# Kernel optimization log

Hardware: AMD Instinct MI355X
Metric: run time of the kernel (lower is better)

Reference implementation:

```python
import jax, jax.numpy as jnp
import numpy as np

RATIO = 2          # Activation1d up_ratio = down_ratio = 2
FIR_K = 12         # up_kernel_size = down_kernel_size = 12
DN = ('NCH', 'OIH', 'NCH')


def kaiser_sinc_filter1d(cutoff, half_width, K):
    # Faithful port of BigVGAN's kaiser_sinc_filter1d (numpy, computed once at setup).
    even = (K % 2 == 0)
    half = K // 2
    delta_f = 4.0 * half_width
    A = 2.285 * (half - 1) * np.pi * delta_f + 7.95
    if A > 50.0:
        beta = 0.1102 * (A - 8.7)
    elif A >= 21.0:
        beta = 0.5842 * (A - 21.0) ** 0.4 + 0.07886 * (A - 21.0)
    else:
        beta = 0.0
    win = np.kaiser(K, beta)  # == torch.kaiser_window(K, beta, periodic=False)
    time = (np.arange(-half, half) + 0.5) if even else (np.arange(K) - half)
    filt = 2.0 * cutoff * win * np.sinc(2.0 * cutoff * time)
    filt = filt / filt.sum()
    return filt.astype(np.float32)


def snake_beta(x, log_alpha, log_beta):
    # SnakeBeta with alpha_logscale=True: x + 1/(beta+eps) * sin(alpha*x)^2
    alpha = jnp.exp(log_alpha)[None, :, None]
    beta = jnp.exp(log_beta)[None, :, None]
    return x + (1.0 / (beta + 1e-9)) * jnp.square(jnp.sin(x * alpha))


def upsample1d(x, filt):
    # UpSample1d: replicate pad, depthwise conv_transpose (stride=ratio), crop.
    C = x.shape[1]
    K = filt.shape[0]
    pad = K // RATIO - 1
    pad_left = pad * RATIO + (K - RATIO) // 2
    pad_right = pad * RATIO + (K - RATIO + 1) // 2
    xp = jnp.pad(x, ((0, 0), (0, 0), (pad, pad)), mode='edge')
    # conv_transpose == correlation with flipped kernel, lhs_dilation=stride, full padding
    w = jnp.broadcast_to(filt[::-1][None, None, :], (C, 1, K))
    y = RATIO * jax.lax.conv_general_dilated(
        xp, w, window_strides=(1,), padding=((K - 1, K - 1),),
        lhs_dilation=(RATIO,), feature_group_count=C, dimension_numbers=DN)
    return y[..., pad_left:-pad_right]  # length = 2*T


def downsample1d(x, filt):
    # DownSample1d / LowPassFilter1d: replicate pad, depthwise strided conv.
    C = x.shape[1]
    K = filt.shape[0]
    even = int(K % 2 == 0)
    pad_left = K // 2 - even
    pad_right = K // 2
    xp = jnp.pad(x, ((0, 0), (0, 0), (pad_left, pad_right)), mode='edge')
    w = jnp.broadcast_to(filt[None, None, :], (C, 1, K))
    return jax.lax.conv_general_dilated(
        xp, w, window_strides=(RATIO,), padding='VALID',
        feature_group_count=C, dimension_numbers=DN)  # length back to T


def activation1d(x, log_alpha, log_beta, up_filt, down_filt):
    return downsample1d(snake_beta(upsample1d(x, up_filt), log_alpha, log_beta), down_filt)


def conv1d_same(x, w, b, dilation):
    K = w.shape[-1]
    pad = (K - 1) * dilation // 2  # get_padding(kernel_size, dilation)
    y = jax.lax.conv_general_dilated(
        x, w, window_strides=(1,), padding=((pad, pad),),
        rhs_dilation=(dilation,), dimension_numbers=DN)
    return y + b[None, :, None]


def setup_inputs() -> dict:
    key = jax.random.key(0)
    ks = jax.random.split(key, 8)
    B, C, T, KSZ = 8, 512, 8192, 3
    x = jax.random.normal(ks[0], (B, C, T), dtype=jnp.float32)
    # SnakeBeta params (logscale init is zeros in torch; small randn for nontrivial grads)
    a1_alpha = 0.2 * jax.random.normal(ks[1], (C,), dtype=jnp.float32)
    a1_beta = 0.2 * jax.random.normal(ks[2], (C,), dtype=jnp.float32)
    a2_alpha = 0.2 * jax.random.normal(ks[3], (C,), dtype=jnp.float32)
    a2_beta = 0.2 * jax.random.normal(ks[4], (C,), dtype=jnp.float32)
    # Conv weights: init_weights -> normal(0, 0.01)
    c1_w = 0.01 * jax.random.normal(ks[5], (C, C, KSZ), dtype=jnp.float32)
    c2_w = 0.01 * jax.random.normal(ks[6], (C, C, KSZ), dtype=jnp.float32)
    c1_b = jnp.zeros((C,), dtype=jnp.float32)
    c2_b = jnp.zeros((C,), dtype=jnp.float32)
    # Kaiser-sinc low-pass FIR (cutoff=0.5/ratio, half_width=0.6/ratio) - fixed buffers
    filt = jnp.asarray(kaiser_sinc_filter1d(0.5 / RATIO, 0.6 / RATIO, FIR_K))
    return {'x': x, 'a1_alpha': a1_alpha, 'a1_beta': a1_beta,
            'a2_alpha': a2_alpha, 'a2_beta': a2_beta,
            'c1_w': c1_w, 'c1_b': c1_b, 'c2_w': c2_w, 'c2_b': c2_b,
            'up_filter': filt, 'down_filter': filt}


def reference(x, a1_alpha, a1_beta, a2_alpha, a2_beta,
              c1_w, c1_b, c2_w, c2_b, up_filter, down_filter):
    # AMPBlock0.forward: single (c1, c2, a1, a2) group; both convs dilation=1.
    xt = activation1d(x, a1_alpha, a1_beta, up_filter, down_filter)
    xt = conv1d_same(xt, c1_w, c1_b, dilation=1)
    xt = activation1d(xt, a2_alpha, a2_beta, up_filter, down_filter)
    xt = conv1d_same(xt, c2_w, c2_b, dilation=1)
    return xt + x  # lengths match, so x[:, :, :xt.shape[2]] == x
```

## Files before the change

kernel.cpp:

```cpp
#include <hip/hip_runtime.h>
#include <cstdint>
#include <cstddef>

#define B_ 8
#define C_ 512
#define T_ 8192

typedef unsigned short ushort_t;
typedef __attribute__((ext_vector_type(8))) short short8;
typedef __attribute__((ext_vector_type(8))) unsigned short ushort8_t;
typedef __attribute__((ext_vector_type(4))) float floatx4;
typedef __attribute__((ext_vector_type(4))) unsigned int uintx4;

__device__ __forceinline__ ushort_t f2bf(float f) {
    unsigned int u = __float_as_uint(f);
    u += 0x7FFFu + ((u >> 16) & 1u);
    return (ushort_t)(u >> 16);
}

#define CT   32
#define TT   128
#define XSTR 148
#define ZSTR 40

__global__ __launch_bounds__(256) void act_t_kernel(
    const float* __restrict__ X,
    const float* __restrict__ la, const float* __restrict__ lb,
    const float* __restrict__ fu, const float* __restrict__ fd,
    ushort_t* __restrict__ Zt)
{
    __shared__ __align__(16) float    xl[CT * XSTR];
    __shared__ __align__(16) ushort_t zs[TT * ZSTR];

    const int t0  = blockIdx.x * TT;
    const int c0  = blockIdx.y * CT;
    const int b   = blockIdx.z;
    const int tid = threadIdx.x;

    const bool interior = (t0 >= 8) && (t0 + 136 <= T_);

    {
        const int row = tid >> 3;
        const int js  = tid & 7;
        const float* Xr = X + ((size_t)b * C_ + c0 + row) * T_;
        if (interior) {
            const float* src = Xr + (t0 - 8);
#pragma unroll
            for (int k = 0; k < 5; ++k) {
                const int seg = js + k * 8;
                if (seg < 36)
                    *(floatx4*)&xl[row * XSTR + seg * 4] = *(const floatx4*)&src[seg * 4];
            }
        } else {
#pragma unroll
            for (int e = 0; e < 18; ++e) {
                const int i = js * 18 + e;
                int t = t0 - 8 + i;
                t = min(max(t, 0), T_ - 1);
                xl[row * XSTR + i] = Xr[t];
            }
        }
    }

    float f[12], g[12];
#pragma unroll
    for (int j = 0; j < 12; ++j) { f[j] = fu[j]; g[j] = fd[j]; }

    const int cl   = tid & 31;
    const int st   = tid >> 5;
    const int st16 = st * 16;
    const int c    = c0 + cl;
    const float alpha = __expf(la[c]);
    const float invb  = 1.0f / (__expf(lb[c]) + 1e-9f);

    __syncthreads();

    float zacc[16];
#pragma unroll
    for (int i = 0; i < 16; ++i) zacc[i] = 0.f;

    if (interior) {
        float xw[32];
#pragma unroll
        for (int i = 0; i < 8; ++i)
            *(floatx4*)&xw[i * 4] = *(const floatx4*)&xl[cl * XSTR + st16 + i * 4];

#pragma unroll
        for (int m = 0; m < 42; ++m) {
            const int h = m >> 1;
            float y = 0.f;
            if (m & 1) {
#pragma unroll
                for (int q = 0; q < 6; ++q) y += xw[3 + h + q] * f[11 - 2 * q];
            } else {
#pragma unroll
                for (int q = 0; q < 6; ++q) y += xw[3 + h + q] * f[10 - 2 * q];
            }
            y *= 2.f;
            const float sn = __sinf(y * alpha);
            y += invb * sn * sn;
            const int dlo = (m >= 11) ? ((m - 10) >> 1) : 0;
            const int dhi = (h < 15) ? h : 15;
#pragma unroll
            for (int dt = dlo; dt <= dhi; ++dt)
                zacc[dt] += g[m - 2 * dt] * y;
        }
    } else {
        const int ts = t0 + st16;
        const float* xr = &xl[cl * XSTR];
#pragma unroll
        for (int m = 0; m < 42; ++m) {
            const int h = m >> 1;
            int n = 2 * ts - 5 + m;
            n = min(max(n, 0), 2 * T_ - 1);
            const int u    = n >> 1;
            const int base = u - (t0 - 8);
            float y = 0.f;
            if (n & 1) {
#pragma unroll
                for (int q = 0; q < 6; ++q) y += xr[base - 2 + q] * f[10 - 2 * q];
            } else {
#pragma unroll
                for (int q = 0; q < 6; ++q) y += xr[base - 3 + q] * f[11 - 2 * q];
            }
            y *= 2.f;
            const float sn = __sinf(y * alpha);
            y += invb * sn * sn;
            const int dlo = (m >= 11) ? ((m - 10) >> 1) : 0;
            const int dhi = (h < 15) ? h : 15;
#pragma unroll
            for (int dt = dlo; dt <= dhi; ++dt)
                zacc[dt] += g[m - 2 * dt] * y;
        }
    }

#pragma unroll
    for (int r = 0; r < 16; ++r)
        zs[(st16 + r) * ZSTR + cl] = f2bf(zacc[r]);

    __syncthreads();

    const int seg = tid & 3;
    const int rr  = tid >> 2;
#pragma unroll
    for (int p = 0; p < 2; ++p) {
        const int row = p * 64 + rr;
        *(uintx4*)&Zt[((size_t)b * T_ + t0 + row) * C_ + c0 + seg * 8] =
            *(const uintx4*)&zs[row * ZSTR + seg * 8];
    }
}

__global__ __launch_bounds__(256) void pack_w_kernel(
    const float* __restrict__ W, ushort_t* __restrict__ Wb)
{
    const int gid   = blockIdx.x * 256 + threadIdx.x;
    const int lane  = gid & 63;
    const int rest  = gid >> 6;
    const int ot    = rest & 31;
    const int chunk = (rest >> 5) & 15;
    const int k     = rest >> 9;
    const int o     = ot * 16 + (lane & 15);
    const int c0    = chunk * 32 + (lane >> 4) * 8;
    ushort8_t v;
#pragma unroll
    for (int j = 0; j < 8; ++j)
        v[j] = f2bf(W[((size_t)o * C_ + c0 + j) * 3 + k]);
    *(ushort8_t*)&Wb[(size_t)gid * 8] = v;
}

__global__ __launch_bounds__(256) void conv_mfma_kernel(
    const ushort_t* __restrict__ Zt,
    const ushort_t* __restrict__ Wb,
    const float* __restrict__ bias,
    const float* __restrict__ resid,
    float* __restrict__ Out,
    const int addResid)
{
    __shared__ __align__(16) ushort_t Al[3 * 8 * 512];
    __shared__ __align__(16) ushort_t Bl[130 * 40];

    const int t0  = blockIdx.x * 128;
    const int o0  = blockIdx.y * 128;
    const int b   = blockIdx.z;
    const int tid = threadIdx.x;
    const int lane = tid & 63;
    const int w    = tid >> 6;
    const int wo   = w & 1;
    const int wt   = w >> 1;

    const ushort_t* zb = Zt + (size_t)b * T_ * C_;

    floatx4 acc[4][4];
#pragma unroll
    for (int i = 0; i < 4; ++i)
#pragma unroll
        for (int j = 0; j < 4; ++j)
            acc[i][j] = (floatx4){0.f, 0.f, 0.f, 0.f};

    const int rB = tid >> 2;
    const int qB = tid & 3;

    for (int chunk = 0; chunk < 16; ++chunk) {
        const int c0 = chunk * 32;

#pragma unroll
        for (int s = 0; s < 6; ++s) {
            const int seg = w * 6 + s;
            const int k   = seg >> 3;
            const int ot8 = seg & 7;
            const ushort_t* gsrc =
                Wb + (size_t)(((k * 16 + chunk) * 32) + (o0 >> 4) + ot8) * 512 + lane * 8;
            __builtin_amdgcn_global_load_lds(
                (const __attribute__((address_space(1))) unsigned int*)gsrc,
                (__attribute__((address_space(3))) unsigned int*)&Al[seg * 512],
                16, 0, 0);
        }

#pragma unroll
        for (int p = 0; p < 3; ++p) {
            const int r = rB + p * 64;
            if (r < 130) {
                const int t = t0 - 1 + r;
                uintx4 v = (uintx4){0u, 0u, 0u, 0u};
                if (t >= 0 && t < T_)
                    v = *(const uintx4*)&zb[(size_t)t * C_ + c0 + qB * 8];
                *(uintx4*)&Bl[r * 40 + qB * 8] = v;
            }
        }
        __syncthreads();

#pragma unroll
        for (int k = 0; k < 3; ++k) {
            short8 af[4], bf[4];
#pragma unroll
            for (int i = 0; i < 4; ++i)
                af[i] = *(const short8*)&Al[(k * 8 + wo * 4 + i) * 512 + lane * 8];
#pragma unroll
            for (int j = 0; j < 4; ++j)
                bf[j] = *(const short8*)&Bl[(wt * 64 + j * 16 + (lane & 15) + k) * 40 + (lane >> 4) * 8];
#pragma unroll
            for (int i = 0; i < 4; ++i)
#pragma unroll
                for (int j = 0; j < 4; ++j)
                    acc[i][j] = __builtin_amdgcn_mfma_f32_16x16x32_bf16(af[i], bf[j], acc[i][j], 0, 0, 0);
        }
        __syncthreads();
    }

    const int tc0 = t0 + wt * 64 + (lane & 15);
#pragma unroll
    for (int i = 0; i < 4; ++i) {
        const int ob = o0 + wo * 64 + i * 16 + (lane >> 4) * 4;
#pragma unroll
        for (int r = 0; r < 4; ++r) {
            const int o = ob + r;
            const float bs = bias[o];
            const size_t rowoff = ((size_t)b * C_ + o) * T_;
#pragma unroll
            for (int j = 0; j < 4; ++j) {
                const int t = tc0 + j * 16;
                float v = acc[i][j][r] + bs;
                if (addResid) v += resid[rowoff + t];
                Out[rowoff + t] = v;
            }
        }
    }
}

extern "C" void kernel_launch(void* const* d_in, const int* in_sizes, int n_in,
                              void* d_out, int out_size, void* d_ws, size_t ws_size,
                              hipStream_t stream)
{
    const float* x   = (const float*)d_in[0];
    const float* a1a = (const float*)d_in[1];
    const float* a1b = (const float*)d_in[2];
    const float* a2a = (const float*)d_in[3];
    const float* a2b = (const float*)d_in[4];
    const float* c1w = (const float*)d_in[5];
    const float* c1b = (const float*)d_in[6];
    const float* c2w = (const float*)d_in[7];
    const float* c2b = (const float*)d_in[8];
    const float* fu  = (const float*)d_in[9];
    const float* fd  = (const float*)d_in[10];
    float* out = (float*)d_out;

    ushort_t* Zt  = (ushort_t*)d_ws;
    float*    y1  = (float*)((char*)d_ws + 67108864);
    ushort_t* Wb1 = (ushort_t*)((char*)d_ws + 67108864 + 134217728);
    ushort_t* Wb2 = Wb1 + 786432;

    dim3 agrid(T_ / TT, C_ / CT, B_);
    dim3 cgrid(T_ / 128, C_ / 128, B_);

    pack_w_kernel<<<384, 256, 0, stream>>>(c1w, Wb1);
    pack_w_kernel<<<384, 256, 0, stream>>>(c2w, Wb2);

    act_t_kernel<<<agrid, 256, 0, stream>>>(x, a1a, a1b, fu, fd, Zt);
    conv_mfma_kernel<<<cgrid, 256, 0, stream>>>(Zt, Wb1, c1b, x, y1, 0);
    act_t_kernel<<<agrid, 256, 0, stream>>>(y1, a2a, a2b, fu, fd, Zt);
    conv_mfma_kernel<<<cgrid, 256, 0, stream>>>(Zt, Wb2, c2b, x, out, 1);
}
```

Measured before the change: 780.5 us.

## Double-buffer activation tile in LDS and stream weights directly into registers

The conv MFMA kernel now double-buffers a 64-channel activation tile in LDS, staged with global_load_lds into an XOR-swizzled layout. The two halo rows are fetched separately. Weight fragments are loaded straight from global memory into registers and ping-ponged, so LDS holds only activations and the next chunk's load overlaps the current MFMAs. Barriers drop from 32 to 8 per block, launch bounds request 3 blocks per CU, and the channel chunk doubles. The cost is more register pressure and uncoalesced-reuse weight reads that now come from global/L2 rather than shared memory.

```diff
diff --git a/kernel.cpp b/kernel.cpp
--- a/kernel.cpp
+++ b/kernel.cpp
@@ -168,7 +168,10 @@
     *(ushort8_t*)&Wb[(size_t)gid * 8] = v;
 }
 
-__global__ __launch_bounds__(256) void conv_mfma_kernel(
+#define BROW 64
+#define BBUF 8320
+
+__global__ __launch_bounds__(256, 3) void conv_mfma_kernel(
     const ushort_t* __restrict__ Zt,
     const ushort_t* __restrict__ Wb,
     const float* __restrict__ bias,
@@ -176,8 +179,7 @@
     float* __restrict__ Out,
     const int addResid)
 {
-    __shared__ __align__(16) ushort_t Al[3 * 8 * 512];
-    __shared__ __align__(16) ushort_t Bl[130 * 40];
+    __shared__ __align__(16) ushort_t Bl[2 * BBUF];
 
     const int t0  = blockIdx.x * 128;
     const int o0  = blockIdx.y * 128;
@@ -197,53 +199,91 @@
         for (int j = 0; j < 4; ++j)
             acc[i][j] = (floatx4){0.f, 0.f, 0.f, 0.f};
 
-    const int rB = tid >> 2;
-    const int qB = tid & 3;
-
-    for (int chunk = 0; chunk < 16; ++chunk) {
-        const int c0 = chunk * 32;
+    const bool ew    = (tid < 16);
+    const int  rr_e  = (tid & 8) ? 129 : 0;
+    const int  seg_e = tid & 7;
+    const int  t_e   = t0 - 1 + rr_e;
+    const bool evld  = ew && (t_e >= 0) && (t_e < T_);
+    const int  ge    = (seg_e ^ (rr_e & 7)) * 8;
+
+    auto loadA = [&](short8 af[4], int cc, int k) {
+        const ushort_t* base =
+            Wb + (size_t)((k * 16 + cc) * 32 + (o0 >> 4) + wo * 4) * 512 + lane * 8;
+#pragma unroll
+        for (int i = 0; i < 4; ++i)
+            af[i] = *(const short8*)(base + i * 512);
+    };
+
+    auto loadB = [&](short8 bf[4], const ushort_t* buf, int k, int cs) {
+        const int cq = cs * 4 + (lane >> 4);
+#pragma unroll
+        for (int j = 0; j < 4; ++j) {
+            const int rr = wt * 64 + j * 16 + (lane & 15) + k;
+            bf[j] = *(const short8*)&buf[rr * BROW + ((cq ^ (rr & 7)) * 8)];
+        }
+    };
+
+    auto stageMain = [&](ushort_t* buf, int cc0) {
+#pragma unroll
+        for (int s4 = 0; s4 < 4; ++s4) {
+            const int row0 = w * 32 + s4 * 8 + 1;
+            const int rr   = row0 + (lane >> 3);
+            const int g    = (lane & 7) ^ (rr & 7);
+            const ushort_t* src = zb + (size_t)(t0 + rr - 1) * C_ + cc0 + g * 8;
+            __builtin_amdgcn_global_load_lds(
+                (const __attribute__((address_space(1))) unsigned int*)src,
+                (__attribute__((address_space(3))) unsigned int*)(buf + row0 * BROW),
+                16, 0, 0);
+        }
+    };
+
+    auto mm16 = [&](short8 af[4], short8 bf[4]) {
+#pragma unroll
+        for (int i = 0; i < 4; ++i)
+#pragma unroll
+            for (int j = 0; j < 4; ++j)
+                acc[i][j] = __builtin_amdgcn_mfma_f32_16x16x32_bf16(
+                    af[i], bf[j], acc[i][j], 0, 0, 0);
+    };
+
+    stageMain(Bl, 0);
+    {
+        uintx4 ev = (uintx4){0u, 0u, 0u, 0u};
+        if (evld) ev = *(const uintx4*)&zb[(size_t)t_e * C_ + ge];
+        if (ew) *(uintx4*)&Bl[rr_e * BROW + seg_e * 8] = ev;
+    }
+    __syncthreads();
+
+    short8 af0[4], af1[4], bf0[4], bf1[4];
+
+    for (int ch = 0; ch < 8; ++ch) {
+        ushort_t* cur = Bl + (ch & 1) * BBUF;
+        ushort_t* nxt = Bl + ((ch + 1) & 1) * BBUF;
+        const int cc0 = ch * 64;
+        const int cc2 = ch * 2;
+
+        loadA(af0, cc2, 0);
+        loadB(bf0, cur, 0, 0);
+
+        uintx4 ev = (uintx4){0u, 0u, 0u, 0u};
 
 #pragma unroll
         for (int s = 0; s < 6; ++s) {
-            const int seg = w * 6 + s;
-            const int k   = seg >> 3;
-            const int ot8 = seg & 7;
-            const ushort_t* gsrc =
-                Wb + (size_t)(((k * 16 + chunk) * 32) + (o0 >> 4) + ot8) * 512 + lane * 8;
-            __builtin_amdgcn_global_load_lds(
-                (const __attribute__((address_space(1))) unsigned int*)gsrc,
-                (__attribute__((address_space(3))) unsigned int*)&Al[seg * 512],
-                16, 0, 0);
-        }
-
-#pragma unroll
-        for (int p = 0; p < 3; ++p) {
-            const int r = rB + p * 64;
-            if (r < 130) {
-                const int t = t0 - 1 + r;
-                uintx4 v = (uintx4){0u, 0u, 0u, 0u};
-                if (t >= 0 && t < T_)
-                    v = *(const uintx4*)&zb[(size_t)t * C_ + c0 + qB * 8];
-                *(uintx4*)&Bl[r * 40 + qB * 8] = v;
-            }
-        }
-        __syncthreads();
-
-#pragma unroll
-        for (int k = 0; k < 3; ++k) {
-            short8 af[4], bf[4];
-#pragma unroll
-            for (int i = 0; i < 4; ++i)
-                af[i] = *(const short8*)&Al[(k * 8 + wo * 4 + i) * 512 + lane * 8];
-#pragma unroll
-            for (int j = 0; j < 4; ++j)
-                bf[j] = *(const short8*)&Bl[(wt * 64 + j * 16 + (lane & 15) + k) * 40 + (lane >> 4) * 8];
-#pragma unroll
-            for (int i = 0; i < 4; ++i)
-#pragma unroll
-                for (int j = 0; j < 4; ++j)
-                    acc[i][j] = __builtin_amdgcn_mfma_f32_16x16x32_bf16(af[i], bf[j], acc[i][j], 0, 0, 0);
-        }
+            const int k1  = (s + 1) >> 1;
+            const int cs1 = (s + 1) & 1;
+            if (s & 1) {
+                if (s < 5) { loadA(af0, cc2 + cs1, k1); loadB(bf0, cur, k1, cs1); }
+            } else {
+                if (s < 5) { loadA(af1, cc2 + cs1, k1); loadB(bf1, cur, k1, cs1); }
+            }
+            if (s == 2 && ch < 7) {
+                stageMain(nxt, cc0 + 64);
+                if (evld) ev = *(const uintx4*)&zb[(size_t)t_e * C_ + cc0 + 64 + ge];
+            }
+            if (s & 1) mm16(af1, bf1);
+            else       mm16(af0, bf0);
+        }
+        if (ch < 7 && ew) *(uintx4*)&nxt[rr_e * BROW + seg_e * 8] = ev;
         __syncthreads();
     }
 
```

Measured after the change: 891.4 us. 1.14x slower.

## Double-buffer conv MFMA LDS tiles with async global_load_lds and swizzled B layout

Applied to the files above, without the earlier changes.

The conv MFMA kernel now double-buffers both the weight and activation tiles in LDS, issuing the loads for the next channel chunk before computing on the current one. Activation tiles are loaded with global_load_lds into an XOR-swizzled, row-paired layout, with edge rows fetched separately by a few threads. This drops one barrier per iteration, aims to hide global load latency behind MFMA work and avoid LDS bank conflicts, and requests two blocks per CU. In exchange it roughly doubles LDS use and adds indexing complexity; the swizzled layout also has to handle the halo rows correctly.

```diff
diff --git a/kernel.cpp b/kernel.cpp
--- a/kernel.cpp
+++ b/kernel.cpp
@@ -168,7 +168,10 @@
     *(ushort8_t*)&Wb[(size_t)gid * 8] = v;
 }
 
-__global__ __launch_bounds__(256) void conv_mfma_kernel(
+#define ABUF 12288
+#define BBUF 4224
+
+__global__ __launch_bounds__(256, 2) void conv_mfma_kernel(
     const ushort_t* __restrict__ Zt,
     const ushort_t* __restrict__ Wb,
     const float* __restrict__ bias,
@@ -176,8 +179,8 @@
     float* __restrict__ Out,
     const int addResid)
 {
-    __shared__ __align__(16) ushort_t Al[3 * 8 * 512];
-    __shared__ __align__(16) ushort_t Bl[130 * 40];
+    __shared__ __align__(16) ushort_t Al[2 * ABUF];
+    __shared__ __align__(16) ushort_t Bs[2 * BBUF];
 
     const int t0  = blockIdx.x * 128;
     const int o0  = blockIdx.y * 128;
@@ -197,54 +200,103 @@
         for (int j = 0; j < 4; ++j)
             acc[i][j] = (floatx4){0.f, 0.f, 0.f, 0.f};
 
-    const int rB = tid >> 2;
-    const int qB = tid & 3;
-
-    for (int chunk = 0; chunk < 16; ++chunk) {
-        const int c0 = chunk * 32;
-
+    int bofs[3][4];
+#pragma unroll
+    for (int k = 0; k < 3; ++k)
+#pragma unroll
+        for (int j = 0; j < 4; ++j) {
+            const int rr = wt * 64 + j * 16 + (lane & 15) + k;
+            const int pr = (rr + 1) >> 1;
+            const int slot = ((((rr + 1) & 1) << 2) | (lane >> 4)) ^ (pr & 7);
+            bofs[k][j] = pr * 64 + slot * 8;
+        }
+
+    const int aoff = wo * 2048 + lane * 8;
+
+    const int prw = 1 + (lane >> 3);
+    const int ub  = (lane & 7) ^ (prw & 7);
+    const int tb0 = t0 + 2 * prw - 2 + (ub >> 2);
+    const int cb0 = (ub & 3) * 8;
+
+    const bool eth = (tid < 8);
+    const int  eq  = tid & 3;
+    const int  ehi = (tid >> 2) & 1;
+    const int  t_e = ehi ? (t0 + 128) : (t0 - 1);
+    const bool evv = eth && (t_e >= 0) && (t_e < T_);
+    const int  edst = ehi ? (65 * 64 + (eq ^ 1) * 8)
+                          : ((4 + eq) * 8);
+    const ushort_t* esrc0 = zb + (size_t)t_e * C_ + eq * 8;
+
+    auto stageA = [&](ushort_t* abuf, int ch) {
 #pragma unroll
         for (int s = 0; s < 6; ++s) {
             const int seg = w * 6 + s;
             const int k   = seg >> 3;
             const int ot8 = seg & 7;
-            const ushort_t* gsrc =
-                Wb + (size_t)(((k * 16 + chunk) * 32) + (o0 >> 4) + ot8) * 512 + lane * 8;
+            const ushort_t* src =
+                Wb + (size_t)(((k * 16 + ch) * 32) + (o0 >> 4) + ot8) * 512 + lane * 8;
             __builtin_amdgcn_global_load_lds(
-                (const __attribute__((address_space(1))) unsigned int*)gsrc,
-                (__attribute__((address_space(3))) unsigned int*)&Al[seg * 512],
+                (const __attribute__((address_space(1))) unsigned int*)src,
+                (__attribute__((address_space(3))) unsigned int*)(abuf + seg * 512),
                 16, 0, 0);
         }
-
-#pragma unroll
-        for (int p = 0; p < 3; ++p) {
-            const int r = rB + p * 64;
-            if (r < 130) {
-                const int t = t0 - 1 + r;
-                uintx4 v = (uintx4){0u, 0u, 0u, 0u};
-                if (t >= 0 && t < T_)
-                    v = *(const uintx4*)&zb[(size_t)t * C_ + c0 + qB * 8];
-                *(uintx4*)&Bl[r * 40 + qB * 8] = v;
-            }
-        }
-        __syncthreads();
+    };
+    auto stageB = [&](ushort_t* bbuf, int ch) {
+#pragma unroll
+        for (int gi = 0; gi < 2; ++gi) {
+            const int G = w * 2 + gi;
+            const ushort_t* src = zb + (size_t)(tb0 + 16 * G) * C_ + ch * 32 + cb0;
+            __builtin_amdgcn_global_load_lds(
+                (const __attribute__((address_space(1))) unsigned int*)src,
+                (__attribute__((address_space(3))) unsigned int*)(bbuf + (1 + 8 * G) * 64),
+                16, 0, 0);
+        }
+    };
+
+    stageA(Al, 0);
+    stageB(Bs, 0);
+    {
+        uintx4 ev = (uintx4){0u, 0u, 0u, 0u};
+        if (evv) ev = *(const uintx4*)esrc0;
+        if (eth) *(uintx4*)&Bs[edst] = ev;
+    }
+    __syncthreads();
+
+#pragma unroll 2
+    for (int ch = 0; ch < 16; ++ch) {
+        ushort_t* curA = Al + (ch & 1) * ABUF;
+        ushort_t* curB = Bs + (ch & 1) * BBUF;
+        ushort_t* nxtA = Al + ((ch + 1) & 1) * ABUF;
+        ushort_t* nxtB = Bs + ((ch + 1) & 1) * BBUF;
+
+        uintx4 ev = (uintx4){0u, 0u, 0u, 0u};
+        if (ch < 15) {
+            stageA(nxtA, ch + 1);
+            stageB(nxtB, ch + 1);
+            if (evv) ev = *(const uintx4*)(esrc0 + (ch + 1) * 32);
+        }
 
 #pragma unroll
         for (int k = 0; k < 3; ++k) {
             short8 af[4], bf[4];
 #pragma unroll
             for (int i = 0; i < 4; ++i)
-                af[i] = *(const short8*)&Al[(k * 8 + wo * 4 + i) * 512 + lane * 8];
+                af[i] = *(const short8*)&curA[aoff + (k * 8 + i) * 512];
 #pragma unroll
             for (int j = 0; j < 4; ++j)
-                bf[j] = *(const short8*)&Bl[(wt * 64 + j * 16 + (lane & 15) + k) * 40 + (lane >> 4) * 8];
+                bf[j] = *(const short8*)&curB[bofs[k][j]];
 #pragma unroll
             for (int i = 0; i < 4; ++i)
 #pragma unroll
                 for (int j = 0; j < 4; ++j)
-                    acc[i][j] = __builtin_amdgcn_mfma_f32_16x16x32_bf16(af[i], bf[j], acc[i][j], 0, 0, 0);
-        }
-        __syncthreads();
+                    acc[i][j] = __builtin_amdgcn_mfma_f32_16x16x32_bf16(
+                        af[i], bf[j], acc[i][j], 0, 0, 0);
+        }
+
+        if (ch < 15) {
+            if (eth) *(uintx4*)&nxtB[edst] = ev;
+            __syncthreads();
+        }
     }
 
     const int tc0 = t0 + wt * 64 + (lane & 15);
```

Measured after the change: 730.6 us. 6.4% less time.

## Double-buffer weight tiles and load activations directly into registers in conv kernel

Applied to the files above, without the earlier changes.

Restructures the MFMA conv kernel so weight tiles are double-buffered in LDS with async global-to-LDS loads for the next channel chunk while the current one computes. The activation (B) operand is no longer staged through LDS; it is read from global memory straight into registers, with prefetch across the three taps and a separate clamped path for edge tiles. It also remaps the 1D grid so blocks land in an XCD-aware order, and raises launch bounds to 3 blocks per SIMD. The aim is to hide memory latency and halve the barriers, at the cost of more uncoalesced direct global loads and extra register pressure.

```diff
diff --git a/kernel.cpp b/kernel.cpp
--- a/kernel.cpp
+++ b/kernel.cpp
@@ -168,7 +168,9 @@
     *(ushort8_t*)&Wb[(size_t)gid * 8] = v;
 }
 
-__global__ __launch_bounds__(256) void conv_mfma_kernel(
+#define ABUF 12288
+
+__global__ __launch_bounds__(256, 3) void conv_mfma_kernel(
     const ushort_t* __restrict__ Zt,
     const ushort_t* __restrict__ Wb,
     const float* __restrict__ bias,
@@ -176,12 +178,15 @@
     float* __restrict__ Out,
     const int addResid)
 {
-    __shared__ __align__(16) ushort_t Al[3 * 8 * 512];
-    __shared__ __align__(16) ushort_t Bl[130 * 40];
-
-    const int t0  = blockIdx.x * 128;
-    const int o0  = blockIdx.y * 128;
-    const int b   = blockIdx.z;
+    __shared__ __align__(16) ushort_t Al[2 * ABUF];
+
+    const int hid = blockIdx.x;
+    const int L   = (hid & 7) * 256 + (hid >> 3);
+    const int b   = L >> 8;
+    const int rem = L & 255;
+    const int t0  = (rem >> 2) * 128;
+    const int o0  = (rem & 3) * 128;
+
     const int tid = threadIdx.x;
     const int lane = tid & 63;
     const int w    = tid >> 6;
@@ -197,54 +202,86 @@
         for (int j = 0; j < 4; ++j)
             acc[i][j] = (floatx4){0.f, 0.f, 0.f, 0.f};
 
-    const int rB = tid >> 2;
-    const int qB = tid & 3;
-
-    for (int chunk = 0; chunk < 16; ++chunk) {
-        const int c0 = chunk * 32;
-
+    const int aoff = wo * 2048 + lane * 8;
+
+    const int  tB   = t0 - 1 + wt * 64 + (lane & 15);
+    const int  cB   = (lane >> 4) * 8;
+    const bool edge = (t0 == 0) || (t0 == T_ - 128);
+    const ushort_t* bbase = zb + (size_t)(edge ? 0 : tB) * C_ + cB;
+
+    auto stageA = [&](ushort_t* abuf, int ch) {
 #pragma unroll
         for (int s = 0; s < 6; ++s) {
             const int seg = w * 6 + s;
             const int k   = seg >> 3;
             const int ot8 = seg & 7;
-            const ushort_t* gsrc =
-                Wb + (size_t)(((k * 16 + chunk) * 32) + (o0 >> 4) + ot8) * 512 + lane * 8;
+            const ushort_t* src =
+                Wb + (size_t)(((k * 16 + ch) * 32) + (o0 >> 4) + ot8) * 512 + lane * 8;
             __builtin_amdgcn_global_load_lds(
-                (const __attribute__((address_space(1))) unsigned int*)gsrc,
-                (__attribute__((address_space(3))) unsigned int*)&Al[seg * 512],
+                (const __attribute__((address_space(1))) unsigned int*)src,
+                (__attribute__((address_space(3))) unsigned int*)(abuf + seg * 512),
                 16, 0, 0);
         }
-
-#pragma unroll
-        for (int p = 0; p < 3; ++p) {
-            const int r = rB + p * 64;
-            if (r < 130) {
-                const int t = t0 - 1 + r;
-                uintx4 v = (uintx4){0u, 0u, 0u, 0u};
-                if (t >= 0 && t < T_)
-                    v = *(const uintx4*)&zb[(size_t)t * C_ + c0 + qB * 8];
-                *(uintx4*)&Bl[r * 40 + qB * 8] = v;
-            }
-        }
-        __syncthreads();
-
-#pragma unroll
-        for (int k = 0; k < 3; ++k) {
-            short8 af[4], bf[4];
-#pragma unroll
-            for (int i = 0; i < 4; ++i)
-                af[i] = *(const short8*)&Al[(k * 8 + wo * 4 + i) * 512 + lane * 8];
+    };
+
+    auto loadB = [&](short8 bf[4], int ch, int k) {
+        if (!edge) {
 #pragma unroll
             for (int j = 0; j < 4; ++j)
-                bf[j] = *(const short8*)&Bl[(wt * 64 + j * 16 + (lane & 15) + k) * 40 + (lane >> 4) * 8];
-#pragma unroll
-            for (int i = 0; i < 4; ++i)
-#pragma unroll
-                for (int j = 0; j < 4; ++j)
-                    acc[i][j] = __builtin_amdgcn_mfma_f32_16x16x32_bf16(af[i], bf[j], acc[i][j], 0, 0, 0);
-        }
-        __syncthreads();
+                bf[j] = *(const short8*)(bbase + (size_t)(ch * 32 + k * 512 + j * 8192));
+        } else {
+            const short8 zv = {0, 0, 0, 0, 0, 0, 0, 0};
+#pragma unroll
+            for (int j = 0; j < 4; ++j) {
+                const int t  = tB + j * 16 + k;
+                const int tc = min(max(t, 0), T_ - 1);
+                short8 v = *(const short8*)&zb[(size_t)tc * C_ + ch * 32 + cB];
+                bf[j] = (t == tc) ? v : zv;
+            }
+        }
+    };
+
+    auto mm16 = [&](short8 af[4], short8 bf[4]) {
+#pragma unroll
+        for (int i = 0; i < 4; ++i)
+#pragma unroll
+            for (int j = 0; j < 4; ++j)
+                acc[i][j] = __builtin_amdgcn_mfma_f32_16x16x32_bf16(
+                    af[i], bf[j], acc[i][j], 0, 0, 0);
+    };
+
+    short8 r0[4], r1[4], r2[4], af[4];
+
+    stageA(Al, 0);
+    loadB(r0, 0, 0);
+    loadB(r1, 0, 1);
+    __syncthreads();
+
+    for (int ch = 0; ch < 16; ++ch) {
+        const ushort_t* curA = Al + (ch & 1) * ABUF;
+        ushort_t* nxtA = Al + ((ch + 1) & 1) * ABUF;
+
+        loadB(r2, ch, 2);
+        if (ch < 15) stageA(nxtA, ch + 1);
+
+#pragma unroll
+        for (int i = 0; i < 4; ++i)
+            af[i] = *(const short8*)&curA[aoff + i * 512];
+        mm16(af, r0);
+        if (ch < 15) loadB(r0, ch + 1, 0);
+
+#pragma unroll
+        for (int i = 0; i < 4; ++i)
+            af[i] = *(const short8*)&curA[aoff + (8 + i) * 512];
+        mm16(af, r1);
+        if (ch < 15) loadB(r1, ch + 1, 1);
+
+#pragma unroll
+        for (int i = 0; i < 4; ++i)
+            af[i] = *(const short8*)&curA[aoff + (16 + i) * 512];
+        mm16(af, r2);
+
+        if (ch < 15) __syncthreads();
     }
 
     const int tc0 = t0 + wt * 64 + (lane & 15);
@@ -290,13 +327,12 @@
     ushort_t* Wb2 = Wb1 + 786432;
 
     dim3 agrid(T_ / TT, C_ / CT, B_);
-    dim3 cgrid(T_ / 128, C_ / 128, B_);
 
     pack_w_kernel<<<384, 256, 0, stream>>>(c1w, Wb1);
     pack_w_kernel<<<384, 256, 0, stream>>>(c2w, Wb2);
 
     act_t_kernel<<<agrid, 256, 0, stream>>>(x, a1a, a1b, fu, fd, Zt);
-    conv_mfma_kernel<<<cgrid, 256, 0, stream>>>(Zt, Wb1, c1b, x, y1, 0);
+    conv_mfma_kernel<<<2048, 256, 0, stream>>>(Zt, Wb1, c1b, x, y1, 0);
     act_t_kernel<<<agrid, 256, 0, stream>>>(y1, a2a, a2b, fu, fd, Zt);
-    conv_mfma_kernel<<<cgrid, 256, 0, stream>>>(Zt, Wb2, c2b, x, out, 1);
-}
+    conv_mfma_kernel<<<2048, 256, 0, stream>>>(Zt, Wb2, c2b, x, out, 1);
+}
```

After: 942.6 us. +20.8%, slower.
